# Optimization experiments

Measured on AMD Instinct MI355X. Metric: run time of the kernel, lower is better.

The kernel has to match this reference:

```python
import math
import jax, jax.numpy as jnp
from jax import lax
import numpy as np

LIDAR_MAX_X = 32.0
LIDAR_MAX_Y = 32.0
NQ = 1280  # eval-branch num_queries hardcoded in the torch module


def sineembed(pos, hidden_dim=256):
    # pos (..., 2) -> (..., hidden_dim); DAB-DETR sine embedding
    half = hidden_dim // 2
    dim_t = 10000.0 ** (2.0 * (jnp.arange(half) // 2).astype(jnp.float32) / half)
    scale = 2.0 * math.pi
    px = (pos[..., 0] * scale)[..., None] / dim_t
    py = (pos[..., 1] * scale)[..., None] / dim_t

    def interleave(p):
        s = jnp.stack([jnp.sin(p[..., 0::2]), jnp.cos(p[..., 1::2])], axis=-1)
        return s.reshape(s.shape[:-2] + (-1,))

    return jnp.concatenate([interleave(py), interleave(px)], axis=-1)


def grid_sample_bilinear_zeros(value, grid):
    # value (B,C,H,W); grid (B,Hg,Wg,2) in [-1,1], (x,y) order,
    # bilinear, padding_mode='zeros', align_corners=False
    B, C, H, W = value.shape
    Hg, Wg = grid.shape[1], grid.shape[2]
    gx = ((grid[..., 0] + 1.0) * 0.5 * W - 0.5).reshape(B, -1)
    gy = ((grid[..., 1] + 1.0) * 0.5 * H - 0.5).reshape(B, -1)
    x0 = jnp.floor(gx)
    y0 = jnp.floor(gy)
    wx1 = gx - x0
    wy1 = gy - y0
    vflat = value.reshape(B, C, H * W)

    def gather(ix, iy, w):
        valid = (ix >= 0) & (ix <= W - 1) & (iy >= 0) & (iy <= H - 1)
        ixc = jnp.clip(ix, 0, W - 1).astype(jnp.int32)
        iyc = jnp.clip(iy, 0, H - 1).astype(jnp.int32)
        idx = iyc * W + ixc  # (B,N)
        v = jnp.take_along_axis(vflat, idx[:, None, :], axis=2)  # (B,C,N)
        return v * (w * valid)[:, None, :]

    out = (gather(x0, y0, (1 - wx1) * (1 - wy1))
           + gather(x0 + 1, y0, wx1 * (1 - wy1))
           + gather(x0, y0 + 1, (1 - wx1) * wy1)
           + gather(x0 + 1, y0 + 1, wx1 * wy1))
    return out.reshape(B, C, Hg, Wg)


def setup_inputs() -> dict:
    key = jax.random.key(0)
    ks = jax.random.split(key, 12)
    B, D, Cin, H, W = 8, 256, 64, 200, 200
    return {
        "queries": jax.random.normal(ks[0], (B, NQ, D), jnp.float32),
        "navi_points": jax.random.normal(ks[1], (B, 2), jnp.float32) * 10.0,
        "bev_feature": jax.random.normal(ks[2], (B, Cin, H, W), jnp.float32),
        "spatial_shape": jnp.array([H, W], jnp.int32),
        "point_score": jax.random.uniform(ks[3], (B, 2), jnp.float32),
        "aw_w": jax.random.normal(ks[4], (1, D), jnp.float32) * 0.02,
        "aw_b": jnp.zeros((1,), jnp.float32),
        "aws_w": jax.random.normal(ks[5], (1, D), jnp.float32) * 0.02,
        "aws_b": jnp.zeros((1,), jnp.float32),
        "conv_w": jax.random.normal(ks[6], (256, Cin, 3, 3), jnp.float32) * 0.02,
        "conv_b": jnp.zeros((256,), jnp.float32),
        "out_w": jax.random.normal(ks[7], (D, D), jnp.float32) * 0.02,
        "out_b": jnp.zeros((D,), jnp.float32),
    }


def reference(queries, navi_points, bev_feature, spatial_shape, point_score,
              aw_w, aw_b, aws_w, aws_b, conv_w, conv_b, out_w, out_b):
    B, nq, D = queries.shape
    # eval branch: expand navi_points to (B, 1280, 1, 2)
    pts = jnp.broadcast_to(navi_points.reshape(B, 1, 1, 2), (B, NQ, 1, 2))
    # normalize then swap -> grid (x=pts_y/max_x, y=pts_x/max_y)
    grid = jnp.stack([pts[..., 1] / LIDAR_MAX_X, pts[..., 0] / LIDAR_MAX_Y], axis=-1)

    # attention weights from queries, softmax over num_points (=1)
    aw = jax.nn.softmax(queries @ aw_w.T + aw_b, axis=-1)  # (B,NQ,1)

    # score weights from sine embedding of point_score
    ps = jnp.broadcast_to(point_score.reshape(B, 1, 1, 2), (B, NQ, 1, 2))
    aws = (sineembed(ps) @ aws_w.T + aws_b).reshape(B, NQ, 1)  # (B,NQ,1)

    # value projection: Conv2d 64->256, 3x3, pad 1, ReLU
    value = lax.conv_general_dilated(bev_feature, conv_w, (1, 1), 'SAME',
                                     dimension_numbers=('NCHW', 'OIHW', 'NCHW'))
    value = jax.nn.relu(value + conv_b[None, :, None, None])

    sampled = grid_sample_bilinear_zeros(value, grid)  # (B,256,NQ,1)

    out = (aw[:, None] * sampled * aws[:, None]).sum(axis=-1)  # (B,256,NQ)
    out = out.transpose(0, 2, 1)  # (B,NQ,256)
    out = out @ out_w.T + out_b
    return out + queries  # dropout is identity at inference
```

## Files before the change

kernel.cpp:

```cpp
#include <hip/hip_runtime.h>
#include <math.h>

#define NQ   1280
#define DD   256
#define CIN  64
#define HH   200
#define WW   200
#define BB   8
#define KW   576
#define TPB  256
#define PER_BLK4 (NQ * DD / 4 / 64)

__device__ __forceinline__ float wave_reduce(float v) {
#pragma unroll
    for (int off = 32; off > 0; off >>= 1) v += __shfl_down(v, off, 64);
    return v;
}

__global__ __launch_bounds__(256) void conv_sample_kernel(
    const float* __restrict__ navi,
    const float* __restrict__ bev,
    const float* __restrict__ pscore,
    const float* __restrict__ aws_w,
    const float* __restrict__ aws_b,
    const float* __restrict__ conv_w,
    const float* __restrict__ conv_b,
    float* __restrict__ s_out,
    float* __restrict__ aws_out)
{
    const int b    = blockIdx.x >> 6;
    const int cgp  = blockIdx.x & 63;
    const int tid  = threadIdx.x;
    const int lane = tid & 63;
    const int wave = tid >> 6;

    __shared__ float win[CIN * 16];
    __shared__ float red[DD];

    float nx = navi[b * 2 + 0];
    float ny = navi[b * 2 + 1];
    float gx = (ny * (1.0f / 32.0f) + 1.0f) * 0.5f * (float)WW - 0.5f;
    float gy = (nx * (1.0f / 32.0f) + 1.0f) * 0.5f * (float)HH - 0.5f;
    float x0f = floorf(gx), y0f = floorf(gy);
    float wx1 = gx - x0f, wy1 = gy - y0f;
    int x0 = (int)x0f, y0 = (int)y0f;

    float cw[4];
    {
        float wx[2] = {1.0f - wx1, wx1};
        float wy[2] = {1.0f - wy1, wy1};
#pragma unroll
        for (int k = 0; k < 4; ++k) {
            int dx = k & 1, dy = k >> 1;
            float ixf = x0f + (float)dx, iyf = y0f + (float)dy;
            bool valid = (ixf >= 0.0f) && (ixf <= (float)(WW - 1)) &&
                         (iyf >= 0.0f) && (iyf <= (float)(HH - 1));
            cw[k] = wx[dx] * wy[dy] * (valid ? 1.0f : 0.0f);
        }
    }

    for (int idx = tid; idx < CIN * 16; idx += TPB) {
        int ci = idx >> 4, pos = idx & 15;
        int yy = y0 - 1 + (pos >> 2);
        int xx = x0 - 1 + (pos & 3);
        float v = 0.0f;
        if (yy >= 0 && yy < HH && xx >= 0 && xx < WW)
            v = bev[((size_t)b * CIN + ci) * (HH * WW) + (size_t)yy * WW + xx];
        win[idx] = v;
    }
    __syncthreads();

    const int c = cgp * 4 + wave;
    const float* wp = conv_w + (size_t)c * KW;
    float a0 = 0.f, a1 = 0.f, a2 = 0.f, a3 = 0.f;
#pragma unroll
    for (int i = 0; i < 9; ++i) {
        int k  = i * 64 + lane;
        int ci = k / 9;
        int r  = k - ci * 9;
        int ky = r / 3;
        int kx = r - ky * 3;
        int base = ci * 16 + ky * 4 + kx;
        float w = wp[k];
        a0 = fmaf(w, win[base],     a0);
        a1 = fmaf(w, win[base + 1], a1);
        a2 = fmaf(w, win[base + 4], a2);
        a3 = fmaf(w, win[base + 5], a3);
    }
    a0 = wave_reduce(a0);
    a1 = wave_reduce(a1);
    a2 = wave_reduce(a2);
    a3 = wave_reduce(a3);
    if (lane == 0) {
        float cb = conv_b[c];
        float v0 = fmaxf(a0 + cb, 0.0f);
        float v1 = fmaxf(a1 + cb, 0.0f);
        float v2 = fmaxf(a2 + cb, 0.0f);
        float v3 = fmaxf(a3 + cb, 0.0f);
        s_out[b * DD + c] = cw[0] * v0 + cw[1] * v1 + cw[2] * v2 + cw[3] * v3;
    }

    if (cgp == 0) {
        float psx = pscore[b * 2 + 0];
        float psy = pscore[b * 2 + 1];
        float p = (tid < 128) ? psy : psx;
        int j = (tid & 127) >> 1;
        float dimt = powf(10000.0f, (float)j * (1.0f / 64.0f));
        float arg = p * 6.283185307179586f / dimt;
        float e = (tid & 1) ? cosf(arg) : sinf(arg);
        red[tid] = e * aws_w[tid];
        __syncthreads();
        for (int off = 128; off > 0; off >>= 1) {
            if (tid < off) red[tid] += red[tid + off];
            __syncthreads();
        }
        if (tid == 0) aws_out[b] = red[0] + aws_b[0];
    }
}

__global__ __launch_bounds__(256) void matvec_add_kernel(
    const float* __restrict__ out_w,
    const float* __restrict__ out_b,
    const float* __restrict__ s_in,
    const float* __restrict__ aws_in,
    const float4* __restrict__ q4,
    float4* __restrict__ out4)
{
    const int b   = blockIdx.x >> 6;
    const int tid = threadIdx.x;

    __shared__ float s_sh[DD];
    __shared__ float t_sh[DD];

    const int base = blockIdx.x * PER_BLK4 + tid;
    float4 qv[PER_BLK4 / TPB];
#pragma unroll
    for (int k = 0; k < PER_BLK4 / TPB; ++k)
        qv[k] = q4[base + k * TPB];

    s_sh[tid] = s_in[b * DD + tid];
    float aws = aws_in[b];
    __syncthreads();

    {
        const float4* wr = (const float4*)(out_w + (size_t)tid * DD);
        const float4* s4 = (const float4*)s_sh;
        float sum = 0.0f;
#pragma unroll
        for (int c4 = 0; c4 < DD / 4; ++c4) {
            float4 w4 = wr[c4];
            float4 sv = s4[c4];
            sum += w4.x * sv.x + w4.y * sv.y + w4.z * sv.z + w4.w * sv.w;
        }
        t_sh[tid] = aws * sum + out_b[tid];
    }
    __syncthreads();

    const float4* t4 = (const float4*)t_sh;
#pragma unroll
    for (int k = 0; k < PER_BLK4 / TPB; ++k) {
        int i = base + k * TPB;
        float4 tv = t4[i & (DD / 4 - 1)];
        float4 v = qv[k];
        v.x += tv.x; v.y += tv.y; v.z += tv.z; v.w += tv.w;
        out4[i] = v;
    }
}

extern "C" void kernel_launch(void* const* d_in, const int* in_sizes, int n_in,
                              void* d_out, int out_size, void* d_ws, size_t ws_size,
                              hipStream_t stream) {
    const float* queries = (const float*)d_in[0];
    const float* navi    = (const float*)d_in[1];
    const float* bev     = (const float*)d_in[2];
    const float* pscore  = (const float*)d_in[4];
    const float* aws_w   = (const float*)d_in[7];
    const float* aws_b   = (const float*)d_in[8];
    const float* conv_w  = (const float*)d_in[9];
    const float* conv_b  = (const float*)d_in[10];
    const float* out_w   = (const float*)d_in[11];
    const float* out_b   = (const float*)d_in[12];

    float* s   = (float*)d_ws;
    float* aws = s + BB * DD;

    conv_sample_kernel<<<BB * 64, TPB, 0, stream>>>(navi, bev, pscore, aws_w,
                                                    aws_b, conv_w, conv_b,
                                                    s, aws);
    matvec_add_kernel<<<BB * 64, TPB, 0, stream>>>(out_w, out_b, s, aws,
                                                   (const float4*)queries,
                                                   (float4*)d_out);
}
```

Baseline: 160.0 us.

## Split matvec from broadcast add and use nontemporal streaming add kernel

```diff
diff --git a/kernel.cpp b/kernel.cpp
--- a/kernel.cpp
+++ b/kernel.cpp
@@ -9,7 +9,8 @@
 #define BB   8
 #define KW   576
 #define TPB  256
-#define PER_BLK4 (NQ * DD / 4 / 64)
+
+typedef float floatx4 __attribute__((ext_vector_type(4)));
 
 __device__ __forceinline__ float wave_reduce(float v) {
 #pragma unroll
@@ -118,53 +119,45 @@
     }
 }
 
-__global__ __launch_bounds__(256) void matvec_add_kernel(
+__global__ __launch_bounds__(256) void matvec_kernel(
     const float* __restrict__ out_w,
     const float* __restrict__ out_b,
     const float* __restrict__ s_in,
     const float* __restrict__ aws_in,
-    const float4* __restrict__ q4,
-    float4* __restrict__ out4)
+    float* __restrict__ t_out)
 {
-    const int b   = blockIdx.x >> 6;
-    const int tid = threadIdx.x;
+    const int b    = blockIdx.x >> 6;
+    const int cgp  = blockIdx.x & 63;
+    const int tid  = threadIdx.x;
+    const int lane = tid & 63;
+    const int wave = tid >> 6;
 
     __shared__ float s_sh[DD];
-    __shared__ float t_sh[DD];
-
-    const int base = blockIdx.x * PER_BLK4 + tid;
-    float4 qv[PER_BLK4 / TPB];
-#pragma unroll
-    for (int k = 0; k < PER_BLK4 / TPB; ++k)
-        qv[k] = q4[base + k * TPB];
-
     s_sh[tid] = s_in[b * DD + tid];
-    float aws = aws_in[b];
     __syncthreads();
 
-    {
-        const float4* wr = (const float4*)(out_w + (size_t)tid * DD);
-        const float4* s4 = (const float4*)s_sh;
-        float sum = 0.0f;
+    const int d = cgp * 4 + wave;
+    const float* wp = out_w + (size_t)d * DD;
+    float sum = 0.0f;
 #pragma unroll
-        for (int c4 = 0; c4 < DD / 4; ++c4) {
-            float4 w4 = wr[c4];
-            float4 sv = s4[c4];
-            sum += w4.x * sv.x + w4.y * sv.y + w4.z * sv.z + w4.w * sv.w;
-        }
-        t_sh[tid] = aws * sum + out_b[tid];
-    }
-    __syncthreads();
+    for (int i = 0; i < 4; ++i)
+        sum = fmaf(wp[i * 64 + lane], s_sh[i * 64 + lane], sum);
+    sum = wave_reduce(sum);
+    if (lane == 0) t_out[b * DD + d] = aws_in[b] * sum + out_b[d];
+}
 
-    const float4* t4 = (const float4*)t_sh;
-#pragma unroll
-    for (int k = 0; k < PER_BLK4 / TPB; ++k) {
-        int i = base + k * TPB;
-        float4 tv = t4[i & (DD / 4 - 1)];
-        float4 v = qv[k];
-        v.x += tv.x; v.y += tv.y; v.z += tv.z; v.w += tv.w;
-        out4[i] = v;
-    }
+__global__ __launch_bounds__(256) void add_kernel(
+    const floatx4* __restrict__ q4,
+    const floatx4* __restrict__ t4,
+    floatx4* __restrict__ out4)
+{
+    const int i = blockIdx.x * TPB + threadIdx.x;
+    floatx4 v = __builtin_nontemporal_load(&q4[i]);
+    const int b  = i / (NQ * DD / 4);
+    const int d4 = i & (DD / 4 - 1);
+    floatx4 tv = t4[b * (DD / 4) + d4];
+    v += tv;
+    __builtin_nontemporal_store(v, &out4[i]);
 }
 
 extern "C" void kernel_launch(void* const* d_in, const int* in_sizes, int n_in,
@@ -183,11 +176,15 @@
 
     float* s   = (float*)d_ws;
     float* aws = s + BB * DD;
+    float* t   = s + BB * DD + 256;
 
     conv_sample_kernel<<<BB * 64, TPB, 0, stream>>>(navi, bev, pscore, aws_w,
                                                     aws_b, conv_w, conv_b,
                                                     s, aws);
-    matvec_add_kernel<<<BB * 64, TPB, 0, stream>>>(out_w, out_b, s, aws,
-                                                   (const float4*)queries,
-                                                   (float4*)d_out);
+    matvec_kernel<<<BB * 64, TPB, 0, stream>>>(out_w, out_b, s, aws, t);
+
+    const int total4 = BB * NQ * DD / 4;
+    add_kernel<<<total4 / TPB, TPB, 0, stream>>>((const floatx4*)queries,
+                                                 (const floatx4*)t,
+                                                 (floatx4*)d_out);
 }
```

Measured after the change: 143.9 us. 10.1% less time.
